# Kernel optimization log

Hardware: AMD Instinct MI355X
Metric: run time of the kernel (lower is better)

Reference implementation:

```python
import math
import jax, jax.numpy as jnp
import numpy as np

B, L, F, H = 16, 1024, 512, 8
D = F // H
FACTOR = 5.0
KEEP_MINLEN = 15.0


def setup_inputs() -> dict:
    key = jax.random.key(0)
    ks = jax.random.split(key, 12)
    inp = {
        "query": jax.random.normal(ks[0], (B, L, F), jnp.float32),
        "key": jax.random.normal(ks[1], (B, L, F), jnp.float32),
        "value": jax.random.normal(ks[2], (B, L, F), jnp.float32),
        "mask": jnp.ones((B, 1, L), jnp.int32),
    }
    s = 0.02
    inp["Wq"] = jax.random.normal(ks[3], (F, F), jnp.float32) * s
    inp["bq"] = jnp.zeros((F,), jnp.float32)
    inp["Wk"] = jax.random.normal(ks[4], (F, F), jnp.float32) * s
    inp["bk"] = jnp.zeros((F,), jnp.float32)
    inp["Wv"] = jax.random.normal(ks[5], (F, F), jnp.float32) * s
    inp["bv"] = jnp.zeros((F,), jnp.float32)
    inp["Wo"] = jax.random.normal(ks[6], (F, F), jnp.float32) * s
    inp["bo"] = jnp.zeros((F,), jnp.float32)
    return inp


def _n_top(Lq: int) -> int:
    if Lq <= KEEP_MINLEN:
        return Lq
    u = int(round(FACTOR * math.ceil(math.log(Lq))))
    return min(u, Lq)


def reference(query, key, value, mask, Wq, bq, Wk, bk, Wv, bv, Wo, bo):
    def proj(x, W, b):
        # torch nn.Linear: x @ W.T + b ; then (B,L,H,D) -> (B,H,L,D)
        return (x @ W.T + b).reshape(B, L, H, D).transpose(0, 2, 1, 3)

    q = proj(query, Wq, bq)
    k = proj(key, Wk, bk)
    v = proj(value, Wv, bv)

    # prob_QK with index=None: full (unscaled) QK to compute sparsity measure M
    scores_full = jnp.einsum('bhqd,bhkd->bhqk', q, k)  # (B,H,L,L)
    M = scores_full.max(-1) - scores_full.mean(-1)      # (B,H,L)
    u = _n_top(L)
    _, idx = jax.lax.top_k(M, u)                        # (B,H,u)

    q_red = jnp.take_along_axis(q, idx[..., None], axis=2)  # (B,H,u,D)
    scores = jnp.einsum('bhud,bhkd->bhuk', q_red, k) / math.sqrt(D)

    neg = (mask == 0)[:, None, :, :]  # (B,1,1,L) broadcasts over heads/queries
    scores = jnp.where(neg, -jnp.inf, scores)
    attn = jax.nn.softmax(scores, axis=-1)
    attn = jnp.where(neg, 0.0, attn)

    ctx_top = jnp.einsum('bhuk,bhkd->bhud', attn, v)   # (B,H,u,D)

    # initial context = mean of V over keys, broadcast to all queries
    context = jnp.broadcast_to(v.mean(axis=2, keepdims=True), (B, H, L, D))
    bi = jnp.arange(B)[:, None, None]
    hi = jnp.arange(H)[None, :, None]
    context = context.at[bi, hi, idx].set(ctx_top)

    x = context.transpose(0, 2, 1, 3).reshape(B, L, H * D)
    return x @ Wo.T + bo
```

## Files before the change

### kernel.cpp

```cpp
#include <hip/hip_runtime.h>
#include <math.h>

#define B_ 16
#define L_ 1024
#define H_ 8
#define U_ 35

typedef float f32x4 __attribute__((ext_vector_type(4)));
typedef short bf16x8 __attribute__((ext_vector_type(8)));

__device__ __forceinline__ unsigned short f2bf(float x) {
    unsigned int u = __float_as_uint(x);
    u += 0x7FFFu + ((u >> 16) & 1u);
    return (unsigned short)(u >> 16);
}
__device__ __forceinline__ float bf2f(unsigned short b) {
    return __uint_as_float(((unsigned int)b) << 16);
}

__device__ __forceinline__ unsigned int cvt_pk_bf16(float a, float b) {
    unsigned int r;
    asm("v_cvt_pk_bf16_f32 %0, %1, %2" : "=v"(r) : "v"(a), "v"(b));
    return r;
}

__device__ __forceinline__ void gl_lds16(const void* g, void* l) {
    __builtin_amdgcn_global_load_lds(
        (const __attribute__((address_space(1))) unsigned int*)g,
        (__attribute__((address_space(3))) unsigned int*)l, 16, 0, 0);
}

#define MFMA(a, b, c) __builtin_amdgcn_mfma_f32_16x16x32_bf16((a), (b), (c), 0, 0, 0)

#define OFF_V      ((size_t)0)
#define OFF_QHI    ((size_t)8388608)
#define OFF_QLO    ((size_t)12582912)
#define OFF_CTXP   OFF_QHI
#define OFF_KHI    ((size_t)16777216)
#define OFF_KLO    ((size_t)20971520)
#define OFF_S      ((size_t)25165824)
#define OFF_WQH    OFF_S
#define OFF_WQL    ((size_t)(OFF_S + 131072))
#define OFF_WKH    ((size_t)(OFF_S + 262144))
#define OFF_WKL    ((size_t)(OFF_S + 393216))
#define OFF_WVH    ((size_t)(OFF_S + 524288))
#define OFF_WVL    ((size_t)(OFF_S + 655360))
#define OFF_M      ((size_t)29753344)
#define OFF_KMEAN  ((size_t)29884416)
#define OFF_VMEAN  ((size_t)29892608)
#define OFF_CTXD   ((size_t)29900800)
#define OFF_IDX    ((size_t)30187520)
#define OFF_OBASE  ((size_t)30192000)

__global__ __launch_bounds__(256) void split_w3(
    const float* __restrict__ Wq, const float* __restrict__ Wk,
    const float* __restrict__ Wv,
    unsigned short* __restrict__ wqh, unsigned short* __restrict__ wql,
    unsigned short* __restrict__ wkh, unsigned short* __restrict__ wkl,
    unsigned short* __restrict__ wvh, unsigned short* __restrict__ wvl)
{
    const int w = blockIdx.x >> 10;
    const int i = (blockIdx.x & 1023) * 256 + threadIdx.x;
    const float* W = (w == 0) ? Wq : (w == 1) ? Wk : Wv;
    unsigned short* hi = (w == 0) ? wqh : (w == 1) ? wkh : wvh;
    unsigned short* lo = (w == 0) ? wql : (w == 1) ? wkl : wvl;
    float x = W[i];
    unsigned short h = f2bf(x);
    hi[i] = h;
    lo[i] = f2bf(x - bf2f(h));
}

__global__ __launch_bounds__(256) void gemm_qkv(
    const float* __restrict__ Aq, const float* __restrict__ Ak,
    const float* __restrict__ Av,
    const unsigned short* __restrict__ wqh, const unsigned short* __restrict__ wql,
    const unsigned short* __restrict__ wkh, const unsigned short* __restrict__ wkl,
    const unsigned short* __restrict__ wvh, const unsigned short* __restrict__ wvl,
    const float* __restrict__ bqp, const float* __restrict__ bkp,
    const float* __restrict__ bvp,
    float* __restrict__ vout,
    unsigned short* __restrict__ qhi_o, unsigned short* __restrict__ qlo_o,
    unsigned short* __restrict__ khi_o, unsigned short* __restrict__ klo_o)
{
    __shared__ __align__(16) unsigned char smem[36864];
    unsigned short (*Ah)[40] = (unsigned short (*)[40])(smem);
    unsigned short (*Al)[40] = (unsigned short (*)[40])(smem + 10240);
    unsigned short (*Bh)[32] = (unsigned short (*)[32])(smem + 20480);
    unsigned short (*Bl)[32] = (unsigned short (*)[32])(smem + 28672);
    float (*Cf)[68] = (float (*)[68])(smem);

    const int z = blockIdx.z;
    const float* A = (z == 0) ? Aq : (z == 1) ? Ak : Av;
    const unsigned short* Whi = (z == 0) ? wqh : (z == 1) ? wkh : wvh;
    const unsigned short* Wlo = (z == 0) ? wql : (z == 1) ? wkl : wvl;
    const float* bias = (z == 0) ? bqp : (z == 1) ? bkp : bvp;
    unsigned short* ohi = (z == 0) ? qhi_o : (z == 1) ? khi_o : nullptr;
    unsigned short* olo = (z == 0) ? qlo_o : (z == 1) ? klo_o : nullptr;

    const int tid = threadIdx.x, lane = tid & 63, wave = tid >> 6;
    const int m0 = blockIdx.x * 128, n0 = blockIdx.y * 128;
    const int wm = (wave >> 1) * 64, wn = (wave & 1) * 64;

    f32x4 zero4 = {0.f, 0.f, 0.f, 0.f};
    f32x4 acc[4][4];
#pragma unroll
    for (int i = 0; i < 4; i++)
#pragma unroll
        for (int j = 0; j < 4; j++) acc[i][j] = zero4;

    const int ar = tid >> 3, ac = (tid & 7) * 4;
    const int kc = (lane >> 4) * 8;
    const int fr = lane & 15;
    const int btr = tid >> 2;
    const int btc = (tid & 3) * 8;
    const int bldsoff = tid * 16;

    for (int k0 = 0; k0 < 512; k0 += 32) {
        if (k0) __syncthreads();
#pragma unroll
        for (int i = 0; i < 2; ++i) {
            size_t gb = (size_t)(n0 + i * 64 + btr) * 512 + k0 + btc;
            gl_lds16(Whi + gb, (unsigned char*)Bh + i * 4096 + bldsoff);
            gl_lds16(Wlo + gb, (unsigned char*)Bl + i * 4096 + bldsoff);
        }
#pragma unroll
        for (int p = 0; p < 4; ++p) {
            float4 a4 = *(const float4*)(A + (size_t)(m0 + ar + p * 32) * 512 + k0 + ac);
            unsigned int h01 = cvt_pk_bf16(a4.x, a4.y);
            unsigned int h23 = cvt_pk_bf16(a4.z, a4.w);
            float r0 = a4.x - __uint_as_float(h01 << 16);
            float r1 = a4.y - __uint_as_float(h01 & 0xFFFF0000u);
            float r2 = a4.z - __uint_as_float(h23 << 16);
            float r3 = a4.w - __uint_as_float(h23 & 0xFFFF0000u);
            unsigned int l01 = cvt_pk_bf16(r0, r1);
            unsigned int l23 = cvt_pk_bf16(r2, r3);
            uint2 hh; hh.x = h01; hh.y = h23;
            uint2 ll; ll.x = l01; ll.y = l23;
            *(uint2*)&Ah[ar + p * 32][ac] = hh;
            *(uint2*)&Al[ar + p * 32][ac] = ll;
        }
        __syncthreads();

        bf16x8 ah[4], al[4];
#pragma unroll
        for (int mi = 0; mi < 4; ++mi) {
            int row = wm + mi * 16 + fr;
            ah[mi] = *(bf16x8*)&Ah[row][kc];
            al[mi] = *(bf16x8*)&Al[row][kc];
        }
#pragma unroll
        for (int ni = 0; ni < 4; ++ni) {
            int rn = wn + ni * 16 + fr;
            bf16x8 bh8 = *(bf16x8*)&Bh[rn][kc];
            bf16x8 bl8 = *(bf16x8*)&Bl[rn][kc];
#pragma unroll
            for (int mi = 0; mi < 4; ++mi) {
                acc[mi][ni] = MFMA(ah[mi], bh8, acc[mi][ni]);
                acc[mi][ni] = MFMA(ah[mi], bl8, acc[mi][ni]);
                acc[mi][ni] = MFMA(al[mi], bh8, acc[mi][ni]);
            }
        }
    }

    const int col = lane & 15, rq = (lane >> 4) * 4;
    const int b_ = m0 >> 10;
    const int l0 = m0 & 1023;

#pragma unroll
    for (int half = 0; half < 2; ++half) {
        __syncthreads();
        if ((wave & 1) == half) {
#pragma unroll
            for (int ni = 0; ni < 4; ++ni) {
                float bn = bias[n0 + half * 64 + ni * 16 + col];
#pragma unroll
                for (int mi = 0; mi < 4; ++mi)
#pragma unroll
                    for (int r = 0; r < 4; ++r)
                        Cf[wm + mi * 16 + rq + r][ni * 16 + col] = acc[mi][ni][r] + bn;
            }
        }
        __syncthreads();
        const int h_ = (n0 >> 6) + half;
        const size_t plane = ((size_t)(b_ * H_ + h_) * L_ + l0) * 64;
        if (z == 2) {
            const int r = tid >> 1, d0 = (tid & 1) * 32;
#pragma unroll
            for (int j = 0; j < 8; ++j) {
                float4 val = *(const float4*)&Cf[r][d0 + j * 4];
                *(float4*)(vout + plane + (size_t)r * 64 + d0 + j * 4) = val;
            }
        } else {
            const int r = tid >> 1, d0 = (tid & 1) * 32;
#pragma unroll
            for (int c = 0; c < 4; ++c) {
                float x[8];
#pragma unroll
                for (int j = 0; j < 8; ++j) x[j] = Cf[r][d0 + c * 8 + j];
                unsigned int h01 = cvt_pk_bf16(x[0], x[1]);
                unsigned int h23 = cvt_pk_bf16(x[2], x[3]);
                unsigned int h45 = cvt_pk_bf16(x[4], x[5]);
                unsigned int h67 = cvt_pk_bf16(x[6], x[7]);
                float r0 = x[0] - __uint_as_float(h01 << 16);
                float r1 = x[1] - __uint_as_float(h01 & 0xFFFF0000u);
                float r2 = x[2] - __uint_as_float(h23 << 16);
                float r3 = x[3] - __uint_as_float(h23 & 0xFFFF0000u);
                float r4 = x[4] - __uint_as_float(h45 << 16);
                float r5 = x[5] - __uint_as_float(h45 & 0xFFFF0000u);
                float r6 = x[6] - __uint_as_float(h67 << 16);
                float r7 = x[7] - __uint_as_float(h67 & 0xFFFF0000u);
                uint4 ph; ph.x = h01; ph.y = h23; ph.z = h45; ph.w = h67;
                uint4 pl;
                pl.x = cvt_pk_bf16(r0, r1);
                pl.y = cvt_pk_bf16(r2, r3);
                pl.z = cvt_pk_bf16(r4, r5);
                pl.w = cvt_pk_bf16(r6, r7);
                *(uint4*)(ohi + plane + (size_t)r * 64 + d0 + c * 8) = ph;
                *(uint4*)(olo + plane + (size_t)r * 64 + d0 + c * 8) = pl;
            }
        }
    }
}

__global__ __launch_bounds__(256) void means_fused(
    const unsigned short* __restrict__ khi, const unsigned short* __restrict__ klo,
    const float* __restrict__ v, float* __restrict__ kmean, float* __restrict__ vmean)
{
    const int which = blockIdx.x >> 7;
    const int bh = blockIdx.x & 127;
    const int d = threadIdx.x & 63, g = threadIdx.x >> 6;
    __shared__ float red[4][64];
    float s = 0.f;
    if (which == 0) {
        size_t base = ((size_t)bh * L_ + g * 256) * 64 + d;
#pragma unroll 8
        for (int l = 0; l < 256; l++) {
            size_t o = base + (size_t)l * 64;
            s += bf2f(khi[o]) + bf2f(klo[o]);
        }
    } else {
        const float* p = v + ((size_t)bh * L_ + g * 256) * 64 + d;
#pragma unroll 8
        for (int l = 0; l < 256; l++) s += p[(size_t)l * 64];
    }
    red[g][d] = s;
    __syncthreads();
    if (threadIdx.x < 64) {
        const int dd = threadIdx.x;
        float m = (red[0][dd] + red[1][dd] + red[2][dd] + red[3][dd]) * (1.0f / 1024.0f);
        (which == 0 ? kmean : vmean)[(size_t)bh * 64 + dd] = m;
    }
}

__global__ __launch_bounds__(256) void qk_rowmax_mfma(
    const unsigned short* __restrict__ qhi, const unsigned short* __restrict__ qlo,
    const unsigned short* __restrict__ khi, const unsigned short* __restrict__ klo,
    const float* __restrict__ kmean, float* __restrict__ Mout)
{
    __shared__ unsigned short Qh[64][72], Ql[64][72];
    __shared__ unsigned short Kh[64][72], Kl[64][72];
    __shared__ float Mred[64][4];
    __shared__ float km[64];
    const int bh = blockIdx.x, q0 = blockIdx.y * 64;
    const int tid = threadIdx.x, lane = tid & 63, wave = tid >> 6;

    if (tid < 64) km[tid] = kmean[bh * 64 + tid];
    {
        int r = tid >> 2, c = (tid & 3) * 16;
        size_t off = ((size_t)bh * L_ + q0 + r) * 64 + c;
        *(uint4*)&Qh[r][c]     = *(const uint4*)(qhi + off);
        *(uint4*)&Qh[r][c + 8] = *(const uint4*)(qhi + off + 8);
        *(uint4*)&Ql[r][c]     = *(const uint4*)(qlo + off);
        *(uint4*)&Ql[r][c + 8] = *(const uint4*)(qlo + off + 8);
    }

    const size_t kb = (size_t)bh * L_ * 64;
    const int sr = tid >> 2, sc = (tid & 3) * 16;
    const int fr = lane & 15;
    f32x4 zero4 = {0.f, 0.f, 0.f, 0.f};

    uint4 pha, phb, pla, plb;
    {
        size_t off = kb + (size_t)sr * 64 + sc;
        pha = *(const uint4*)(khi + off);  phb = *(const uint4*)(khi + off + 8);
        pla = *(const uint4*)(klo + off);  plb = *(const uint4*)(klo + off + 8);
    }

    __syncthreads();

    bf16x8 qah[2][4], qal[2][4];
#pragma unroll
    for (int ks = 0; ks < 2; ++ks) {
        int kcol = ks * 32 + (lane >> 4) * 8;
#pragma unroll
        for (int mi = 0; mi < 4; ++mi) {
            qah[ks][mi] = *(bf16x8*)&Qh[mi * 16 + fr][kcol];
            qal[ks][mi] = *(bf16x8*)&Ql[mi * 16 + fr][kcol];
        }
    }

    float rmax[4][4];
#pragma unroll
    for (int mi = 0; mi < 4; ++mi)
#pragma unroll
        for (int r = 0; r < 4; ++r) rmax[mi][r] = -INFINITY;

    for (int kt = 0; kt < 16; ++kt) {
        if (kt) __syncthreads();
        *(uint4*)&Kh[sr][sc] = pha;  *(uint4*)&Kh[sr][sc + 8] = phb;
        *(uint4*)&Kl[sr][sc] = pla;  *(uint4*)&Kl[sr][sc + 8] = plb;
        __syncthreads();

        if (kt < 15) {
            size_t off = kb + (size_t)((kt + 1) * 64 + sr) * 64 + sc;
            pha = *(const uint4*)(khi + off);  phb = *(const uint4*)(khi + off + 8);
            pla = *(const uint4*)(klo + off);  plb = *(const uint4*)(klo + off + 8);
        }

        f32x4 acc[4];
#pragma unroll
        for (int mi = 0; mi < 4; ++mi) acc[mi] = zero4;

#pragma unroll
        for (int ks = 0; ks < 2; ++ks) {
            int kcol = ks * 32 + (lane >> 4) * 8;
            int krow = wave * 16 + fr;
            bf16x8 bh8 = *(bf16x8*)&Kh[krow][kcol];
            bf16x8 bl8 = *(bf16x8*)&Kl[krow][kcol];
#pragma unroll
            for (int mi = 0; mi < 4; ++mi) {
                acc[mi] = MFMA(qah[ks][mi], bh8, acc[mi]);
                acc[mi] = MFMA(qah[ks][mi], bl8, acc[mi]);
                acc[mi] = MFMA(qal[ks][mi], bh8, acc[mi]);
            }
        }
#pragma unroll
        for (int mi = 0; mi < 4; ++mi)
#pragma unroll
            for (int r = 0; r < 4; ++r)
                rmax[mi][r] = fmaxf(rmax[mi][r], acc[mi][r]);
    }

#pragma unroll
    for (int mi = 0; mi < 4; ++mi)
#pragma unroll
        for (int r = 0; r < 4; ++r) {
            float v = rmax[mi][r];
            v = fmaxf(v, __shfl_xor(v, 1));
            v = fmaxf(v, __shfl_xor(v, 2));
            v = fmaxf(v, __shfl_xor(v, 4));
            v = fmaxf(v, __shfl_xor(v, 8));
            rmax[mi][r] = v;
        }
    if ((lane & 15) == 0) {
        int quad = lane >> 4;
#pragma unroll
        for (int mi = 0; mi < 4; ++mi)
#pragma unroll
            for (int r = 0; r < 4; ++r)
                Mred[mi * 16 + quad * 4 + r][wave] = rmax[mi][r];
    }
    __syncthreads();
    if (tid < 64) {
        float mx = fmaxf(fmaxf(Mred[tid][0], Mred[tid][1]),
                         fmaxf(Mred[tid][2], Mred[tid][3]));
        float dot = 0.f;
#pragma unroll 4
        for (int d = 0; d < 64; ++d)
            dot = fmaf(bf2f(Qh[tid][d]) + bf2f(Ql[tid][d]), km[d], dot);
        Mout[(size_t)bh * L_ + q0 + tid] = mx - dot;
    }
}

__global__ __launch_bounds__(256) void topk35(
    const float* __restrict__ Min, int* __restrict__ idx_out)
{
    const int bh = blockIdx.x;
    const int tid = threadIdx.x;
    __shared__ float vals[1024];
    __shared__ float wv[4];
    __shared__ int wi[4];
    for (int i = tid; i < 1024; i += 256) vals[i] = Min[(size_t)bh * 1024 + i];
    __syncthreads();
    for (int it = 0; it < U_; ++it) {
        float bv = -INFINITY; int bi = 1 << 30;
        for (int i = tid; i < 1024; i += 256) {
            float x = vals[i];
            if (x > bv) { bv = x; bi = i; }
        }
#pragma unroll
        for (int off = 32; off; off >>= 1) {
            float ov = __shfl_down(bv, off);
            int   oi = __shfl_down(bi, off);
            if (ov > bv || (ov == bv && oi < bi)) { bv = ov; bi = oi; }
        }
        if ((tid & 63) == 0) { wv[tid >> 6] = bv; wi[tid >> 6] = bi; }
        __syncthreads();
        if (tid == 0) {
#pragma unroll
            for (int w = 1; w < 4; ++w) {
                if (wv[w] > bv || (wv[w] == bv && wi[w] < bi)) { bv = wv[w]; bi = wi[w]; }
            }
            idx_out[bh * U_ + it] = bi;
            vals[bi] = -INFINITY;
        }
        __syncthreads();
    }
}

__global__ __launch_bounds__(256) void scores_red(
    const unsigned short* __restrict__ qhi, const unsigned short* __restrict__ qlo,
    const unsigned short* __restrict__ khi, const unsigned short* __restrict__ klo,
    const int* __restrict__ idx, const int* __restrict__ mask,
    float* __restrict__ S)
{
    __shared__ float Qs[64][36];
    __shared__ float Ks[64][68];
    const int bh = blockIdx.x;
    const int b = bh >> 3;
    const int tid = threadIdx.x;
    const int tk = tid & 63, tg = tid >> 6;

    for (int t = tid; t < 36 * 64; t += 256) {
        int u = t >> 6, d = t & 63;
        float val = 0.f;
        if (u < U_) {
            int l = idx[bh * U_ + u];
            size_t off = ((size_t)bh * L_ + l) * 64 + d;
            val = bf2f(qhi[off]) + bf2f(qlo[off]);
        }
        Qs[d][u] = val;
    }

    const size_t kb = (size_t)bh * L_ * 64;
    const int sr = tid >> 2, sc = (tid & 3) * 16;
    float acc[9];
    const int kt0 = blockIdx.y * 2;
    for (int ki = 0; ki < 2; ++ki) {
        int kt = kt0 + ki;
        if (ki) __syncthreads();
        {
            size_t off = kb + (size_t)(kt * 64 + sr) * 64 + sc;
            uint4 h0 = *(const uint4*)(khi + off);
            uint4 h1 = *(const uint4*)(khi + off + 8);
            uint4 l0 = *(const uint4*)(klo + off);
            uint4 l1 = *(const uint4*)(klo + off + 8);
            unsigned short hv[16], lv[16];
            *(uint4*)hv = h0; *(uint4*)(hv + 8) = h1;
            *(uint4*)lv = l0; *(uint4*)(lv + 8) = l1;
#pragma unroll
            for (int i = 0; i < 16; ++i)
                Ks[sc + i][sr] = bf2f(hv[i]) + bf2f(lv[i]);
        }
        __syncthreads();
#pragma unroll
        for (int j = 0; j < 9; j++) acc[j] = 0.f;
#pragma unroll 4
        for (int d = 0; d < 64; ++d) {
            float kv = Ks[d][tk];
#pragma unroll
            for (int j = 0; j < 9; j++) acc[j] = fmaf(Qs[d][tg + 4 * j], kv, acc[j]);
        }
        const int kcol = kt * 64 + tk;
        const bool msk = (mask[b * L_ + kcol] == 0);
#pragma unroll
        for (int j = 0; j < 9; j++) {
            int u = tg + 4 * j;
            if (u < U_)
                S[((size_t)bh * U_ + u) * 1024 + kcol] = msk ? -INFINITY : acc[j] * 0.125f;
        }
    }
}

__global__ __launch_bounds__(256) void softmax_rows(float* __restrict__ S)
{
    const size_t base = (size_t)blockIdx.x * 1024;
    const int tid = threadIdx.x;
    __shared__ float redm[4];
    __shared__ float reds[4];
    float4 v = *(const float4*)(S + base + tid * 4);
    float mx = fmaxf(fmaxf(v.x, v.y), fmaxf(v.z, v.w));
#pragma unroll
    for (int off = 32; off; off >>= 1) mx = fmaxf(mx, __shfl_down(mx, off));
    if ((tid & 63) == 0) redm[tid >> 6] = mx;
    __syncthreads();
    mx = fmaxf(fmaxf(redm[0], redm[1]), fmaxf(redm[2], redm[3]));
    float e0 = __expf(v.x - mx), e1 = __expf(v.y - mx);
    float e2 = __expf(v.z - mx), e3 = __expf(v.w - mx);
    float s = e0 + e1 + e2 + e3;
#pragma unroll
    for (int off = 32; off; off >>= 1) s += __shfl_down(s, off);
    if ((tid & 63) == 0) reds[tid >> 6] = s;
    __syncthreads();
    s = reds[0] + reds[1] + reds[2] + reds[3];
    const float inv = 1.0f / s;
    float4 o; o.x = e0 * inv; o.y = e1 * inv; o.z = e2 * inv; o.w = e3 * inv;
    *(float4*)(S + base + tid * 4) = o;
}

__global__ __launch_bounds__(256) void ctx_partial(
    const float* __restrict__ S, const float* __restrict__ v,
    float* __restrict__ ctxp)
{
    __shared__ float Vs[128][68];
    __shared__ float Wt[36][128];
    const int bh = blockIdx.x, kc = blockIdx.y;
    const int tid = threadIdx.x;
    const int td = tid & 63, tg = tid >> 6;
    const int lr = tid >> 2, lc0 = (tid & 3) * 16;

    const float* vbase = v + ((size_t)bh * L_ + kc * 128) * 64;
    const float* Sbase = S + (size_t)bh * U_ * 1024 + kc * 128;

#pragma unroll
    for (int hh = 0; hh < 2; ++hh) {
        int row = lr + hh * 64;
        const float* src = vbase + (size_t)row * 64 + lc0;
        *(float4*)&Vs[row][lc0 + 0]  = *(const float4*)(src + 0);
        *(float4*)&Vs[row][lc0 + 4]  = *(const float4*)(src + 4);
        *(float4*)&Vs[row][lc0 + 8]  = *(const float4*)(src + 8);
        *(float4*)&Vs[row][lc0 + 12] = *(const float4*)(src + 12);
    }
    for (int t = tid; t < 36 * 128; t += 256) {
        int u = t >> 7, kk = t & 127;
        Wt[u][kk] = (u < U_) ? Sbase[(size_t)u * 1024 + kk] : 0.f;
    }
    __syncthreads();

    float acc[9];
#pragma unroll
    for (int j = 0; j < 9; j++) acc[j] = 0.f;
#pragma unroll 2
    for (int kk = 0; kk < 128; ++kk) {
        float vv = Vs[kk][td];
#pragma unroll
        for (int j = 0; j < 9; j++) acc[j] = fmaf(Wt[tg + 4 * j][kk], vv, acc[j]);
    }
#pragma unroll
    for (int j = 0; j < 9; j++) {
        int u = tg + 4 * j;
        if (u < U_)
            ctxp[((size_t)(kc * 128 + bh) * 36 + u) * 64 + td] = acc[j];
    }
}

__global__ __launch_bounds__(256) void ctx_reduce_diff(
    const float* __restrict__ ctxp, const float* __restrict__ vmean,
    float* __restrict__ ctxd)
{
    const int i = blockIdx.x * 256 + threadIdx.x;
    const int d = i & 63;
    const int rest = i >> 6;
    const int u = rest % U_;
    const int bh = rest / U_;
    float s = 0.f;
#pragma unroll
    for (int kc = 0; kc < 8; ++kc)
        s += ctxp[((size_t)(kc * 128 + bh) * 36 + u) * 64 + d];
    ctxd[i] = s - vmean[(size_t)bh * 64 + d];
}

__global__ __launch_bounds__(256) void vmean_proj(
    const float* __restrict__ vmean, const float* __restrict__ Wo,
    const float* __restrict__ bo, float* __restrict__ obase)
{
    const int b = blockIdx.x >> 3, n0 = (blockIdx.x & 7) * 64;
    const int tid = threadIdx.x;
    __shared__ float xbar[512];
    __shared__ float psum[64][5];
    for (int i = tid; i < 512; i += 256)
        xbar[i] = vmean[(size_t)(b * 8 + (i >> 6)) * 64 + (i & 63)];
    __syncthreads();
    const int n = n0 + (tid >> 2), fq = (tid & 3) * 128;
    float s = 0.f;
    for (int f = 0; f < 128; f += 4) {
        float4 w = *(const float4*)(Wo + (size_t)n * 512 + fq + f);
        s += xbar[fq + f] * w.x + xbar[fq + f + 1] * w.y +
             xbar[fq + f + 2] * w.z + xbar[fq + f + 3] * w.w;
    }
    psum[tid >> 2][tid & 3] = s;
    __syncthreads();
    if (tid < 64)
        obase[(size_t)b * 512 + n0 + tid] =
            psum[tid][0] + psum[tid][1] + psum[tid][2] + psum[tid][3] + bo[n0 + tid];
}

__global__ void broadcast_out(const float* __restrict__ obase, float* __restrict__ out)
{
    const size_t e = ((size_t)blockIdx.x * 256 + threadIdx.x) * 4;
    const int n = (int)(e & 511);
    const int b = (int)(e >> 19);
    *(float4*)(out + e) = *(const float4*)(obase + (b << 9) + n);
}

__global__ __launch_bounds__(128) void delta_out(
    const float* __restrict__ ctxd, const int* __restrict__ idx,
    const float* __restrict__ Wo, float* __restrict__ out)
{
    const int bh = blockIdx.x, b = bh >> 3, h = bh & 7;
    const int tid = threadIdx.x;
    const int n = blockIdx.y * 128 + tid;
    __shared__ float sd[U_][64];
    __shared__ int ls[U_];
    if (tid < U_) ls[tid] = idx[bh * U_ + tid];
    for (int t = tid; t < U_ * 64; t += 128)
        sd[t >> 6][t & 63] = ctxd[(size_t)bh * U_ * 64 + t];

    float4 w[16];
    const float* wp = Wo + (size_t)n * 512 + h * 64;
#pragma unroll
    for (int jc = 0; jc < 16; ++jc) w[jc] = *(const float4*)(wp + jc * 4);
    __syncthreads();

    for (int u = 0; u < U_; ++u) {
        float acc = 0.f;
#pragma unroll
        for (int jc = 0; jc < 16; ++jc) {
            float4 dv = *(const float4*)&sd[u][jc * 4];
            acc = fmaf(dv.w, w[jc].w, fmaf(dv.z, w[jc].z,
                  fmaf(dv.y, w[jc].y, fmaf(dv.x, w[jc].x, acc))));
        }
        atomicAdd(out + ((size_t)b * L_ + ls[u]) * 512 + n, acc);
    }
}

extern "C" void kernel_launch(void* const* d_in, const int* in_sizes, int n_in,
                              void* d_out, int out_size, void* d_ws, size_t ws_size,
                              hipStream_t stream)
{
    (void)in_sizes; (void)n_in; (void)out_size; (void)ws_size;
    const float* query = (const float*)d_in[0];
    const float* key   = (const float*)d_in[1];
    const float* value = (const float*)d_in[2];
    const int*   mask  = (const int*)d_in[3];
    const float* Wq = (const float*)d_in[4];
    const float* bq = (const float*)d_in[5];
    const float* Wk = (const float*)d_in[6];
    const float* bk = (const float*)d_in[7];
    const float* Wv = (const float*)d_in[8];
    const float* bvp = (const float*)d_in[9];
    const float* Wo = (const float*)d_in[10];
    const float* bo = (const float*)d_in[11];
    float* out = (float*)d_out;

    float* ws = (float*)d_ws;
    float* v      = ws + OFF_V;
    unsigned short* q_hi = (unsigned short*)(ws + OFF_QHI);
    unsigned short* q_lo = (unsigned short*)(ws + OFF_QLO);
    unsigned short* k_hi = (unsigned short*)(ws + OFF_KHI);
    unsigned short* k_lo = (unsigned short*)(ws + OFF_KLO);
    float* ctxp   = ws + OFF_CTXP;
    float* S      = ws + OFF_S;
    float* Marr   = ws + OFF_M;
    float* kmean  = ws + OFF_KMEAN;
    float* vmean  = ws + OFF_VMEAN;
    float* ctxd   = ws + OFF_CTXD;
    int*   idx    = (int*)(ws + OFF_IDX);
    float* obase  = ws + OFF_OBASE;
    unsigned short* wqh = (unsigned short*)(ws + OFF_WQH);
    unsigned short* wql = (unsigned short*)(ws + OFF_WQL);
    unsigned short* wkh = (unsigned short*)(ws + OFF_WKH);
    unsigned short* wkl = (unsigned short*)(ws + OFF_WKL);
    unsigned short* wvh = (unsigned short*)(ws + OFF_WVH);
    unsigned short* wvl = (unsigned short*)(ws + OFF_WVL);

    split_w3<<<3072, 256, 0, stream>>>(Wq, Wk, Wv, wqh, wql, wkh, wkl, wvh, wvl);

    gemm_qkv<<<dim3(128, 4, 3), 256, 0, stream>>>(
        query, key, value,
        wqh, wql, wkh, wkl, wvh, wvl,
        bq, bk, bvp,
        v, q_hi, q_lo, k_hi, k_lo);

    means_fused<<<256, 256, 0, stream>>>(k_hi, k_lo, v, kmean, vmean);
    vmean_proj<<<128, 256, 0, stream>>>(vmean, Wo, bo, obase);

    qk_rowmax_mfma<<<dim3(128, 16), 256, 0, stream>>>(q_hi, q_lo, k_hi, k_lo, kmean, Marr);
    topk35<<<128, 256, 0, stream>>>(Marr, idx);

    scores_red<<<dim3(128, 8), 256, 0, stream>>>(q_hi, q_lo, k_hi, k_lo, idx, mask, S);
    softmax_rows<<<B_ * H_ * U_, 256, 0, stream>>>(S);
    ctx_partial<<<dim3(128, 8), 256, 0, stream>>>(S, v, ctxp);
    ctx_reduce_diff<<<1120, 256, 0, stream>>>(ctxp, vmean, ctxd);

    broadcast_out<<<8192, 256, 0, stream>>>(obase, out);
    delta_out<<<dim3(128, 4), 128, 0, stream>>>(ctxd, idx, Wo, out);
}
```

Baseline: 449.5 us.

## Double-buffer K tiles via direct LDS loads and swizzle B/K shared layouts

In the QKV projection GEMM, the A-tile global loads are prefetched into registers one k-step ahead, and the weight tiles in shared memory use an XOR-swizzled column layout to avoid bank conflicts. In the QK row-max kernel, the register-staged K tiles are replaced by direct global-to-LDS loads into a double buffer, also swizzled, which removes one barrier per iteration and overlaps the next tile's load with the current MFMAs. This costs extra register pressure from the A prefetch and doubles the K shared-memory footprint, which may reduce occupancy.

```diff
diff --git a/kernel.cpp b/kernel.cpp
--- a/kernel.cpp
+++ b/kernel.cpp
@@ -85,8 +85,8 @@
     __shared__ __align__(16) unsigned char smem[36864];
     unsigned short (*Ah)[40] = (unsigned short (*)[40])(smem);
     unsigned short (*Al)[40] = (unsigned short (*)[40])(smem + 10240);
-    unsigned short (*Bh)[32] = (unsigned short (*)[32])(smem + 20480);
-    unsigned short (*Bl)[32] = (unsigned short (*)[32])(smem + 28672);
+    unsigned char* Bh = smem + 20480;
+    unsigned char* Bl = smem + 28672;
     float (*Cf)[68] = (float (*)[68])(smem);
 
     const int z = blockIdx.z;
@@ -112,20 +112,25 @@
     const int kc = (lane >> 4) * 8;
     const int fr = lane & 15;
     const int btr = tid >> 2;
-    const int btc = (tid & 3) * 8;
+    const int btc = ((tid & 3) ^ ((tid >> 2) & 3)) * 8;
     const int bldsoff = tid * 16;
+
+    float4 areg[4];
+#pragma unroll
+    for (int p = 0; p < 4; ++p)
+        areg[p] = *(const float4*)(A + (size_t)(m0 + ar + p * 32) * 512 + ac);
 
     for (int k0 = 0; k0 < 512; k0 += 32) {
         if (k0) __syncthreads();
 #pragma unroll
         for (int i = 0; i < 2; ++i) {
             size_t gb = (size_t)(n0 + i * 64 + btr) * 512 + k0 + btc;
-            gl_lds16(Whi + gb, (unsigned char*)Bh + i * 4096 + bldsoff);
-            gl_lds16(Wlo + gb, (unsigned char*)Bl + i * 4096 + bldsoff);
+            gl_lds16(Whi + gb, Bh + i * 4096 + bldsoff);
+            gl_lds16(Wlo + gb, Bl + i * 4096 + bldsoff);
         }
 #pragma unroll
         for (int p = 0; p < 4; ++p) {
-            float4 a4 = *(const float4*)(A + (size_t)(m0 + ar + p * 32) * 512 + k0 + ac);
+            float4 a4 = areg[p];
             unsigned int h01 = cvt_pk_bf16(a4.x, a4.y);
             unsigned int h23 = cvt_pk_bf16(a4.z, a4.w);
             float r0 = a4.x - __uint_as_float(h01 << 16);
@@ -140,6 +145,11 @@
             *(uint2*)&Al[ar + p * 32][ac] = ll;
         }
         __syncthreads();
+        if (k0 + 32 < 512) {
+#pragma unroll
+            for (int p = 0; p < 4; ++p)
+                areg[p] = *(const float4*)(A + (size_t)(m0 + ar + p * 32) * 512 + k0 + 32 + ac);
+        }
 
         bf16x8 ah[4], al[4];
 #pragma unroll
@@ -151,8 +161,9 @@
 #pragma unroll
         for (int ni = 0; ni < 4; ++ni) {
             int rn = wn + ni * 16 + fr;
-            bf16x8 bh8 = *(bf16x8*)&Bh[rn][kc];
-            bf16x8 bl8 = *(bf16x8*)&Bl[rn][kc];
+            int bb = rn * 64 + ((kc * 2) ^ ((rn & 3) << 4));
+            bf16x8 bh8 = *(bf16x8*)(Bh + bb);
+            bf16x8 bl8 = *(bf16x8*)(Bl + bb);
 #pragma unroll
             for (int mi = 0; mi < 4; ++mi) {
                 acc[mi][ni] = MFMA(ah[mi], bh8, acc[mi][ni]);
@@ -258,7 +269,7 @@
     const float* __restrict__ kmean, float* __restrict__ Mout)
 {
     __shared__ unsigned short Qh[64][72], Ql[64][72];
-    __shared__ unsigned short Kh[64][72], Kl[64][72];
+    __shared__ __align__(16) unsigned char Kp[2][2][8192];
     __shared__ float Mred[64][4];
     __shared__ float km[64];
     const int bh = blockIdx.x, q0 = blockIdx.y * 64;
@@ -275,18 +286,22 @@
     }
 
     const size_t kb = (size_t)bh * L_ * 64;
-    const int sr = tid >> 2, sc = (tid & 3) * 16;
+    const int srow = tid >> 3;
+    const int scol = ((tid & 7) ^ ((tid >> 3) & 7)) * 8;
+    const int sdst = tid * 16;
+
+    {
+        size_t g0 = kb + (size_t)(srow) * 64 + scol;
+        size_t g1 = kb + (size_t)(32 + srow) * 64 + scol;
+        gl_lds16(khi + g0, &Kp[0][0][sdst]);
+        gl_lds16(khi + g1, &Kp[0][0][4096 + sdst]);
+        gl_lds16(klo + g0, &Kp[0][1][sdst]);
+        gl_lds16(klo + g1, &Kp[0][1][4096 + sdst]);
+    }
+    __syncthreads();
+
     const int fr = lane & 15;
     f32x4 zero4 = {0.f, 0.f, 0.f, 0.f};
-
-    uint4 pha, phb, pla, plb;
-    {
-        size_t off = kb + (size_t)sr * 64 + sc;
-        pha = *(const uint4*)(khi + off);  phb = *(const uint4*)(khi + off + 8);
-        pla = *(const uint4*)(klo + off);  plb = *(const uint4*)(klo + off + 8);
-    }
-
-    __syncthreads();
 
     bf16x8 qah[2][4], qal[2][4];
 #pragma unroll
@@ -305,16 +320,20 @@
 #pragma unroll
         for (int r = 0; r < 4; ++r) rmax[mi][r] = -INFINITY;
 
+    const int krow = wave * 16 + fr;
+    const int kbase = krow * 128;
+    const int kxor = (krow & 7) << 4;
+
     for (int kt = 0; kt < 16; ++kt) {
-        if (kt) __syncthreads();
-        *(uint4*)&Kh[sr][sc] = pha;  *(uint4*)&Kh[sr][sc + 8] = phb;
-        *(uint4*)&Kl[sr][sc] = pla;  *(uint4*)&Kl[sr][sc + 8] = plb;
-        __syncthreads();
-
+        const int cur = kt & 1;
         if (kt < 15) {
-            size_t off = kb + (size_t)((kt + 1) * 64 + sr) * 64 + sc;
-            pha = *(const uint4*)(khi + off);  phb = *(const uint4*)(khi + off + 8);
-            pla = *(const uint4*)(klo + off);  plb = *(const uint4*)(klo + off + 8);
+            const int nb = cur ^ 1;
+            size_t g0 = kb + (size_t)((kt + 1) * 64 + srow) * 64 + scol;
+            size_t g1 = g0 + (size_t)32 * 64;
+            gl_lds16(khi + g0, &Kp[nb][0][sdst]);
+            gl_lds16(khi + g1, &Kp[nb][0][4096 + sdst]);
+            gl_lds16(klo + g0, &Kp[nb][1][sdst]);
+            gl_lds16(klo + g1, &Kp[nb][1][4096 + sdst]);
         }
 
         f32x4 acc[4];
@@ -323,10 +342,9 @@
 
 #pragma unroll
         for (int ks = 0; ks < 2; ++ks) {
-            int kcol = ks * 32 + (lane >> 4) * 8;
-            int krow = wave * 16 + fr;
-            bf16x8 bh8 = *(bf16x8*)&Kh[krow][kcol];
-            bf16x8 bl8 = *(bf16x8*)&Kl[krow][kcol];
+            int byte = kbase + (((ks * 32 + (lane >> 4) * 8) * 2) ^ kxor);
+            bf16x8 bh8 = *(bf16x8*)&Kp[cur][0][byte];
+            bf16x8 bl8 = *(bf16x8*)&Kp[cur][1][byte];
 #pragma unroll
             for (int mi = 0; mi < 4; ++mi) {
                 acc[mi] = MFMA(qah[ks][mi], bh8, acc[mi]);
@@ -339,6 +357,8 @@
 #pragma unroll
             for (int r = 0; r < 4; ++r)
                 rmax[mi][r] = fmaxf(rmax[mi][r], acc[mi][r]);
+
+        __syncthreads();
     }
 
 #pragma unroll
```

Measured after the change: 435.4 us. 3.1% less time.
